# Performance work log

Hardware: AMD Instinct MI355X
Metric: run time of the kernel (lower is better)

The kernel has to match this reference:

```python
import jax, jax.numpy as jnp
import numpy as np

H = W = 512
P = H * W          # total superpixel member pixels
N_SP = 1024        # number of superpixels


def _conv(x, w, b):
    # x: [N,C,H,W], w: [O,I,3,3] -> [N,O,H,W], SAME padding
    y = jax.lax.conv_general_dilated(
        x, w, window_strides=(1, 1), padding='SAME',
        dimension_numbers=('NCHW', 'OIHW', 'NCHW'))
    return y + b[None, :, None, None]


def _embed(raw, w1, b1, w2, b2, w3, b3):
    h = jax.nn.relu(_conv(raw, w1, b1))
    h = jax.nn.relu(_conv(h, w2, b2))
    return _conv(h, w3, b3)  # [1, 10, H, W]


def setup_inputs() -> dict:
    key = jax.random.key(0)
    ks = jax.random.split(key, 6)
    raw = jax.random.normal(ks[0], (1, 1, H, W), dtype=jnp.float32)
    w1 = jax.random.normal(ks[1], (64, 1, 3, 3), dtype=jnp.float32) * 0.3
    b1 = jnp.zeros((64,), jnp.float32)
    w2 = jax.random.normal(ks[2], (64, 64, 3, 3), dtype=jnp.float32) * 0.05
    b2 = jnp.zeros((64,), jnp.float32)
    w3 = jax.random.normal(ks[3], (10, 64, 3, 3), dtype=jnp.float32) * 0.05
    b3 = jnp.zeros((10,), jnp.float32)
    pix_rc = jax.random.randint(ks[4], (P, 2), 0, H, dtype=jnp.int32)
    seg_ids = jax.random.randint(ks[5], (P,), 0, N_SP, dtype=jnp.int32)
    return {"raw": raw, "w1": w1, "b1": b1, "w2": w2, "b2": b2,
            "w3": w3, "b3": b3, "pix_rc": pix_rc, "seg_ids": seg_ids,
            "n_sp": N_SP}


def reference(raw, w1, b1, w2, b2, w3, b3, pix_rc, seg_ids, n_sp):
    feats = _embed(raw, w1, b1, w2, b2, w3, b3)  # [1, C, H, W]
    f = feats[0]                                  # [C, H, W]
    # gather per-pixel feature vectors: [P, C]
    vals = f[:, pix_rc[:, 0], pix_rc[:, 1]].T
    # scatter-mean over superpixels (= per-sp sum / mass)
    sums = jax.ops.segment_sum(vals, seg_ids, num_segments=n_sp)      # [n_sp, C]
    cnts = jax.ops.segment_sum(jnp.ones((vals.shape[0],), vals.dtype),
                               seg_ids, num_segments=n_sp)            # [n_sp]
    return sums / jnp.maximum(cnts, 1.0)[:, None]
```

## Files before the change

### kernel.cpp

```cpp
#include <hip/hip_runtime.h>

typedef __attribute__((ext_vector_type(8))) short short8;
typedef __attribute__((ext_vector_type(4))) float f32x4;

constexpr int H = 512, W = 512;
constexpr int P = H * W;
constexpr int NSP = 1024;
constexpr int SBLK = 512;
constexpr int FGRP = 16;

__device__ inline unsigned short f2bf(float f) {
  unsigned u = __builtin_bit_cast(unsigned, f);
  unsigned r = (u + 0x7fffu + ((u >> 16) & 1u)) >> 16;
  return (unsigned short)r;
}
__device__ inline float bflo(unsigned u) { return __builtin_bit_cast(float, u << 16); }
__device__ inline float bfhi(unsigned u) { return __builtin_bit_cast(float, u & 0xffff0000u); }

__device__ inline int xcd_swz(int b, int cpx) { return (b & 7) * cpx + (b >> 3); }

__global__ __launch_bounds__(256) void prep_k(const float* __restrict__ w2,
                                              const float* __restrict__ w3,
                                              unsigned short* __restrict__ wt2s,
                                              unsigned short* __restrict__ wt3s,
                                              unsigned short* __restrict__ zeros) {
  if (blockIdx.x == 0 && threadIdx.x < 128) zeros[threadIdx.x] = 0;
  int i = blockIdx.x * 256 + threadIdx.x;
  if (i < 36864) {
    int k = i >> 11;
    int t = (i >> 3) & 255;
    int e = i & 7;
    int r = t >> 2, sp = t & 3, s = sp ^ ((r >> 2) & 3);
    int tap = k >> 1, ic = (k & 1) * 32 + s * 8 + e;
    wt2s[i] = f2bf(w2[r * 576 + ic * 9 + tap]);
  } else if (i < 46080) {
    int j = i - 36864;
    int k = j >> 9;
    int t = (j >> 3) & 63;
    int e = j & 7;
    int r = t >> 2, sp = t & 3, s = sp ^ ((r >> 2) & 3);
    int tap = k >> 1, ic = (k & 1) * 32 + s * 8 + e;
    wt3s[j] = (r < 10) ? f2bf(w3[r * 576 + ic * 9 + tap]) : (unsigned short)0;
  }
}

__global__ __launch_bounds__(512) void conv2_k(const float* __restrict__ raw,
                                               const float* __restrict__ w1,
                                               const float* __restrict__ b1,
                                               const unsigned short* __restrict__ wts,
                                               const float* __restrict__ bias,
                                               unsigned short* __restrict__ ynhwc) {
  constexpr int DCS = 4096;
  __shared__ __align__(16) unsigned short acts[352 * 64];
  __shared__ __align__(16) unsigned short wbuf[3 * DCS];
  __shared__ unsigned short rawtb[12 * 36 + 4];
  int tid = threadIdx.x;
  int lane = tid & 63, wave = tid >> 6;
  int logical = xcd_swz(blockIdx.x, 128);
  int tilex = logical & 15, tiley = logical >> 4;
  int c0 = tilex * 32, r0 = tiley * 8;

#pragma unroll
  for (int k0 = 0; k0 < 2; ++k0) {
    const unsigned short* src = wts + (size_t)k0 * DCS + tid * 8;
    unsigned short* dstb = wbuf + k0 * DCS + wave * 512;
    __builtin_amdgcn_global_load_lds((const __attribute__((address_space(1))) void*)src,
                                     (__attribute__((address_space(3))) void*)dstb, 16, 0, 0);
  }
  if (tid < 432) {
    int rr = tid / 36, cc = tid - rr * 36;
    int gr = r0 + rr - 2, gc = c0 + cc - 2;
    bool ok = ((unsigned)gr < 512u) && ((unsigned)gc < 512u);
    rawtb[tid] = ok ? f2bf(raw[gr * 512 + gc]) : (unsigned short)0;
  }

  int q = lane >> 4, n = lane & 15;
  int og1 = wave & 3;
  short8 a1f;
  {
    short av[8];
#pragma unroll
    for (int e = 0; e < 8; ++e) av[e] = 0;
    int oc = og1 * 16 + n;
    if (q == 0) {
#pragma unroll
      for (int e = 0; e < 8; ++e) av[e] = (short)f2bf(w1[oc * 9 + e]);
    } else if (q == 1) {
      av[0] = (short)f2bf(w1[oc * 9 + 8]);
    }
    a1f = (short8){av[0], av[1], av[2], av[3], av[4], av[5], av[6], av[7]};
  }
  float bb1[4];
#pragma unroll
  for (int r2 = 0; r2 < 4; ++r2) bb1[r2] = b1[og1 * 16 + q * 4 + r2];
  __syncthreads();

  char* actw = (char*)acts;
  int tbase = (wave < 4) ? 0 : 11;
  for (int ti = 0; ti < 11; ++ti) {
    int t = tbase + ti;
    int px = t * 16 + n;
    bool okp = px < 340;
    int prow = px / 34, pcol = px - prow * 34;
    int prc = okp ? prow : 9;
    short bv[8];
#pragma unroll
    for (int e = 0; e < 8; ++e) bv[e] = 0;
    if (q == 0) {
#pragma unroll
      for (int e = 0; e < 8; ++e) {
        int dy = e / 3, dx = e - dy * 3;
        bv[e] = (short)rawtb[(prc + dy) * 36 + pcol + dx];
      }
    } else if (q == 1) {
      bv[0] = (short)rawtb[(prc + 2) * 36 + pcol + 2];
    }
    short8 b1f = (short8){bv[0], bv[1], bv[2], bv[3], bv[4], bv[5], bv[6], bv[7]};
    f32x4 d = __builtin_amdgcn_mfma_f32_16x16x32_bf16(a1f, b1f,
                                                       (f32x4){0.f, 0.f, 0.f, 0.f}, 0, 0, 0);
    int gr1 = r0 + prow - 1, gc1 = c0 + pcol - 1;
    bool ok1 = okp && ((unsigned)gr1 < 512u) && ((unsigned)gc1 < 512u);
    float o0 = ok1 ? fmaxf(d.x + bb1[0], 0.f) : 0.f;
    float o1 = ok1 ? fmaxf(d.y + bb1[1], 0.f) : 0.f;
    float o2 = ok1 ? fmaxf(d.z + bb1[2], 0.f) : 0.f;
    float o3 = ok1 ? fmaxf(d.w + bb1[3], 0.f) : 0.f;
    unsigned lo = (unsigned)f2bf(o0) | ((unsigned)f2bf(o1) << 16);
    unsigned hi = (unsigned)f2bf(o2) | ((unsigned)f2bf(o3) << 16);
    int wa = px * 128 + ((((og1 * 2 + (q >> 1)) ^ (px & 7)) << 4)) + ((q & 1) << 3);
    *reinterpret_cast<uint2*>(actw + wa) = make_uint2(lo, hi);
  }
  __syncthreads();

  f32x4 acc[4][2];
#pragma unroll
  for (int og = 0; og < 4; ++og)
#pragma unroll
    for (int g = 0; g < 2; ++g) acc[og][g] = (f32x4){0.f, 0.f, 0.f, 0.f};

  int plbase[2];
#pragma unroll
  for (int g = 0; g < 2; ++g) plbase[g] = wave * 34 + 16 * g + n;
  const char* actb = (const char*)acts;

#pragma unroll
  for (int j = 0; j < 9; ++j) {
    if (j == 8) {
      asm volatile("s_waitcnt vmcnt(0)" ::: "memory");
    } else {
      asm volatile("s_waitcnt vmcnt(1)" ::: "memory");
    }
    __builtin_amdgcn_sched_barrier(0);
    __builtin_amdgcn_s_barrier();
    __builtin_amdgcn_sched_barrier(0);
    if (j + 2 < 9) {
      const unsigned short* src = wts + (size_t)(j + 2) * DCS + tid * 8;
      unsigned short* dstb = wbuf + ((j + 2) % 3) * DCS + wave * 512;
      __builtin_amdgcn_global_load_lds((const __attribute__((address_space(1))) void*)src,
                                       (__attribute__((address_space(3))) void*)dstb, 16, 0, 0);
    }
    const int kyy = j / 3, kxx = j - kyy * 3;
    const char* sb = (const char*)(wbuf + (j % 3) * DCS);
#pragma unroll
    for (int kc = 0; kc < 2; ++kc) {
      const char* wb = sb + kc * 4096;
      short8 af[4];
#pragma unroll
      for (int og = 0; og < 4; ++og) {
        int r = og * 16 + n;
        af[og] = *reinterpret_cast<const short8*>(wb + r * 64 + ((q ^ ((r >> 2) & 3)) * 16));
      }
#pragma unroll
      for (int g = 0; g < 2; ++g) {
        int pl = plbase[g] + kyy * 34 + kxx;
        int addr = pl * 128 + (((kc * 4 + q) ^ (pl & 7)) * 16);
        short8 bf = *reinterpret_cast<const short8*>(actb + addr);
#pragma unroll
        for (int og = 0; og < 4; ++og)
          acc[og][g] = __builtin_amdgcn_mfma_f32_16x16x32_bf16(af[og], bf, acc[og][g], 0, 0, 0);
      }
    }
  }

  __syncthreads();
  char* ob = (char*)acts;
#pragma unroll
  for (int og = 0; og < 4; ++og) {
    float b0 = bias[og * 16 + q * 4 + 0], b1v = bias[og * 16 + q * 4 + 1];
    float b2 = bias[og * 16 + q * 4 + 2], b3 = bias[og * 16 + q * 4 + 3];
#pragma unroll
    for (int g = 0; g < 2; ++g) {
      int pl = wave * 32 + g * 16 + n;
      f32x4 v = acc[og][g];
      float o0 = fmaxf(v.x + b0, 0.f), o1 = fmaxf(v.y + b1v, 0.f);
      float o2 = fmaxf(v.z + b2, 0.f), o3 = fmaxf(v.w + b3, 0.f);
      unsigned lo = (unsigned)f2bf(o0) | ((unsigned)f2bf(o1) << 16);
      unsigned hi = (unsigned)f2bf(o2) | ((unsigned)f2bf(o3) << 16);
      int lslot = og * 2 + (q >> 1);
      int wa = pl * 128 + (((lslot ^ (pl & 7)) << 4)) + ((q & 1) << 3);
      *reinterpret_cast<uint2*>(ob + wa) = make_uint2(lo, hi);
    }
  }
  __syncthreads();
  char* yb = (char*)ynhwc;
#pragma unroll
  for (int it = 0; it < 4; ++it) {
    int c = it * 512 + tid;
    int pl = c >> 3, slot = c & 7;
    uint4 v = *reinterpret_cast<const uint4*>(ob + pl * 128 + ((slot ^ (pl & 7)) << 4));
    size_t gb = (((size_t)(r0 + (pl >> 5)) * 512) + c0 + (pl & 31)) * 128 + slot * 16;
    *reinterpret_cast<uint4*>(yb + gb) = v;
  }
}

__global__ __launch_bounds__(512) void conv3_k(const unsigned short* __restrict__ xin,
                                               const unsigned short* __restrict__ wts,
                                               const float* __restrict__ bias,
                                               unsigned short* __restrict__ feats,
                                               const unsigned short* __restrict__ zeros) {
  __shared__ __align__(16) unsigned short acts[352 * 64];
  __shared__ __align__(16) unsigned short wl[9216];
  int tid = threadIdx.x;
  int lane = tid & 63, wave = tid >> 6;
  int logical = xcd_swz(blockIdx.x, 128);
  int tilex = logical & 15, tiley = logical >> 4;
  int c0 = tilex * 32, r0 = tiley * 8;

  for (int wi = wave; wi < 18; wi += 8) {
    const unsigned short* src = wts + (size_t)wi * 512 + lane * 8;
    unsigned short* dstb = &wl[wi * 512];
    __builtin_amdgcn_global_load_lds((const __attribute__((address_space(1))) void*)src,
                                     (__attribute__((address_space(3))) void*)dstb, 16, 0, 0);
  }
  for (int wi = wave; wi < 44; wi += 8) {
    int cidx = wi * 64 + lane;
    int pix = cidx >> 3, slotp = cidx & 7;
    int prow = pix / 34, pcol = pix - prow * 34;
    int gr = r0 + prow - 1, gc = c0 + pcol - 1;
    int slot = slotp ^ (pix & 7);
    bool ok = (pix < 340) & ((unsigned)gr < 512u) & ((unsigned)gc < 512u);
    const unsigned short* src = ok ? (xin + (((size_t)(gr * 512 + gc)) << 6) + slot * 8) : zeros;
    unsigned short* dstb = &acts[wi * 512];
    __builtin_amdgcn_global_load_lds((const __attribute__((address_space(1))) void*)src,
                                     (__attribute__((address_space(3))) void*)dstb, 16, 0, 0);
  }
  __syncthreads();

  int q = lane >> 4, n = lane & 15;
  f32x4 acc[2];
#pragma unroll
  for (int g = 0; g < 2; ++g) acc[g] = (f32x4){0.f, 0.f, 0.f, 0.f};
  int plbase[2];
#pragma unroll
  for (int g = 0; g < 2; ++g) plbase[g] = wave * 34 + 16 * g + n;
  const char* actb = (const char*)acts;
  const char* wb0 = (const char*)wl;

#pragma unroll
  for (int k = 0; k < 18; ++k) {
    const int tap = k >> 1, kc = k & 1;
    const int kyy = tap / 3, kxx = tap - kyy * 3;
    short8 af = *reinterpret_cast<const short8*>(wb0 + k * 1024 + n * 64 +
                                                 ((q ^ ((n >> 2) & 3)) * 16));
#pragma unroll
    for (int g = 0; g < 2; ++g) {
      int pl = plbase[g] + kyy * 34 + kxx;
      int addr = pl * 128 + (((kc * 4 + q) ^ (pl & 7)) * 16);
      short8 bf = *reinterpret_cast<const short8*>(actb + addr);
      acc[g] = __builtin_amdgcn_mfma_f32_16x16x32_bf16(af, bf, acc[g], 0, 0, 0);
    }
  }

  __syncthreads();
  char* ob = (char*)acts;
  float bb[4];
#pragma unroll
  for (int r2 = 0; r2 < 4; ++r2) {
    int oc = q * 4 + r2;
    bb[r2] = (oc < 10) ? bias[oc] : 0.f;
  }
#pragma unroll
  for (int g = 0; g < 2; ++g) {
    int pl = wave * 32 + g * 16 + n;
    f32x4 v = acc[g];
    float o0 = v.x + bb[0], o1 = v.y + bb[1], o2 = v.z + bb[2], o3 = v.w + bb[3];
    if (q < 2) {
      unsigned u0 = (unsigned)f2bf(o0) | ((unsigned)f2bf(o1) << 16);
      unsigned u1 = (unsigned)f2bf(o2) | ((unsigned)f2bf(o3) << 16);
      *reinterpret_cast<uint2*>(ob + pl * 24 + q * 8) = make_uint2(u0, u1);
    } else if (q == 2) {
      *reinterpret_cast<unsigned*>(ob + pl * 24 + 16) =
          (unsigned)f2bf(o0) | ((unsigned)f2bf(o1) << 16);
    }
  }
  __syncthreads();
  char* fb = (char*)feats;
#pragma unroll
  for (int it = 0; it < 3; ++it) {
    int c = it * 512 + tid;
    if (c < 1280) {
      int row = c / 160, wb = c - row * 160;
      int byte = wb * 4;
      int px = byte / 20, off = byte - px * 20;
      unsigned v = *reinterpret_cast<const unsigned*>(ob + (row * 32 + px) * 24 + off);
      size_t gbyte = (((size_t)(r0 + row) * 512) + c0) * 20 + (size_t)byte;
      *reinterpret_cast<unsigned*>(fb + gbyte) = v;
    }
  }
}

__global__ __launch_bounds__(512) void scatter_k(const unsigned short* __restrict__ feats,
                                                 const int* __restrict__ pix_rc,
                                                 const int* __restrict__ seg,
                                                 float* __restrict__ partials) {
  __shared__ float ls[NSP * 10];
  __shared__ float lc[NSP];
  int tid = threadIdx.x;
  for (int i = tid; i < NSP * 10; i += 512) ls[i] = 0.f;
  for (int i = tid; i < NSP; i += 512) lc[i] = 0.f;
  __syncthreads();

  constexpr int PER = P / SBLK;
  int p0 = blockIdx.x * PER;
  for (int p = p0 + tid; p < p0 + PER; p += 512) {
    int2 rc = *reinterpret_cast<const int2*>(pix_rc + 2 * p);
    int s = seg[p];
    size_t gpix = (size_t)rc.x * 512 + rc.y;
    const char* fp = (const char*)feats + gpix * 20;
    uint4 a = *reinterpret_cast<const uint4*>(fp);
    unsigned e = *reinterpret_cast<const unsigned*>(fp + 16);
    float v[10];
    v[0] = bflo(a.x); v[1] = bfhi(a.x);
    v[2] = bflo(a.y); v[3] = bfhi(a.y);
    v[4] = bflo(a.z); v[5] = bfhi(a.z);
    v[6] = bflo(a.w); v[7] = bfhi(a.w);
    v[8] = bflo(e);   v[9] = bfhi(e);
#pragma unroll
    for (int ch = 0; ch < 10; ++ch) atomicAdd(&ls[s * 10 + ch], v[ch]);
    atomicAdd(&lc[s], 1.f);
  }
  __syncthreads();

  float* outp = partials + (size_t)blockIdx.x * (NSP * 11);
  for (int i = tid; i < NSP * 10; i += 512) outp[i] = ls[i];
  for (int i = tid; i < NSP; i += 512) outp[NSP * 10 + i] = lc[i];
}

__global__ __launch_bounds__(256) void finA_k(const float* __restrict__ partials,
                                              float* __restrict__ partials2) {
  int g = blockIdx.x / 44;
  int e = (blockIdx.x - g * 44) * 256 + threadIdx.x;
  const float* base = partials + (size_t)(g * 32) * (NSP * 11) + e;
  float s = 0.f;
#pragma unroll 8
  for (int k = 0; k < 32; ++k) s += base[(size_t)k * (NSP * 11)];
  partials2[(size_t)g * (NSP * 11) + e] = s;
}

__global__ __launch_bounds__(256) void finB_k(const float* __restrict__ partials2,
                                              float* __restrict__ out) {
  int i = blockIdx.x * 256 + threadIdx.x;
  if (i >= NSP * 10) return;
  int sp = i / 10;
  float s = 0.f, cnt = 0.f;
#pragma unroll
  for (int g = 0; g < FGRP; ++g) {
    const float* pp = partials2 + (size_t)g * (NSP * 11);
    s += pp[i];
    cnt += pp[NSP * 10 + sp];
  }
  out[i] = s / fmaxf(cnt, 1.f);
}

extern "C" void kernel_launch(void* const* d_in, const int* in_sizes, int n_in,
                              void* d_out, int out_size, void* d_ws, size_t ws_size,
                              hipStream_t stream) {
  const float* raw = (const float*)d_in[0];
  const float* w1  = (const float*)d_in[1];
  const float* b1  = (const float*)d_in[2];
  const float* w2  = (const float*)d_in[3];
  const float* b2  = (const float*)d_in[4];
  const float* w3  = (const float*)d_in[5];
  const float* b3  = (const float*)d_in[6];
  const int* pix_rc = (const int*)d_in[7];
  const int* seg    = (const int*)d_in[8];
  float* out = (float*)d_out;

  char* ws = (char*)d_ws;
  float* partials  = (float*)(ws + 0);
  float* partials2 = (float*)(ws + 23068672);
  unsigned short* h2    = (unsigned short*)(ws + 25165824);
  unsigned short* feats = (unsigned short*)(ws + 58720256);
  unsigned short* wt2s  = (unsigned short*)(ws + 63963136);
  unsigned short* wt3s  = (unsigned short*)(ws + 64036864);
  unsigned short* zeros = (unsigned short*)(ws + 64055296);

  prep_k<<<180, 256, 0, stream>>>(w2, w3, wt2s, wt3s, zeros);
  conv2_k<<<1024, 512, 0, stream>>>(raw, w1, b1, wt2s, b2, h2);
  conv3_k<<<1024, 512, 0, stream>>>(h2, wt3s, b3, feats, zeros);
  scatter_k<<<SBLK, 512, 0, stream>>>(feats, pix_rc, seg, partials);
  finA_k<<<FGRP * 44, 256, 0, stream>>>(partials, partials2);
  finB_k<<<40, 256, 0, stream>>>(partials2, out);
}
```

Before: 80.25 us.

## Read conv weights directly from global memory instead of staging in LDS

Removes the LDS weight buffers and the triple-buffered async weight pipeline, including its per-tap barriers, in both conv kernels. Each wave now loads its MFMA A-fragments straight from global memory, and the prep kernel drops the XOR swizzle since no LDS bank layout is needed. It also raises launch bounds to a minimum of 6 blocks per CU, using the freed LDS to fit more resident blocks. The cost is redundant global/L2 weight reads by every wave, with latency exposed in the MFMA loop, and possible register pressure from the occupancy hint.

```diff
diff --git a/kernel.cpp b/kernel.cpp
--- a/kernel.cpp
+++ b/kernel.cpp
@@ -30,7 +30,7 @@
     int k = i >> 11;
     int t = (i >> 3) & 255;
     int e = i & 7;
-    int r = t >> 2, sp = t & 3, s = sp ^ ((r >> 2) & 3);
+    int r = t >> 2, s = t & 3;
     int tap = k >> 1, ic = (k & 1) * 32 + s * 8 + e;
     wt2s[i] = f2bf(w2[r * 576 + ic * 9 + tap]);
   } else if (i < 46080) {
@@ -38,21 +38,19 @@
     int k = j >> 9;
     int t = (j >> 3) & 63;
     int e = j & 7;
-    int r = t >> 2, sp = t & 3, s = sp ^ ((r >> 2) & 3);
+    int r = t >> 2, s = t & 3;
     int tap = k >> 1, ic = (k & 1) * 32 + s * 8 + e;
     wt3s[j] = (r < 10) ? f2bf(w3[r * 576 + ic * 9 + tap]) : (unsigned short)0;
   }
 }
 
-__global__ __launch_bounds__(512) void conv2_k(const float* __restrict__ raw,
-                                               const float* __restrict__ w1,
-                                               const float* __restrict__ b1,
-                                               const unsigned short* __restrict__ wts,
-                                               const float* __restrict__ bias,
-                                               unsigned short* __restrict__ ynhwc) {
-  constexpr int DCS = 4096;
+__global__ __launch_bounds__(512, 6) void conv2_k(const float* __restrict__ raw,
+                                                  const float* __restrict__ w1,
+                                                  const float* __restrict__ b1,
+                                                  const unsigned short* __restrict__ wts,
+                                                  const float* __restrict__ bias,
+                                                  unsigned short* __restrict__ ynhwc) {
   __shared__ __align__(16) unsigned short acts[352 * 64];
-  __shared__ __align__(16) unsigned short wbuf[3 * DCS];
   __shared__ unsigned short rawtb[12 * 36 + 4];
   int tid = threadIdx.x;
   int lane = tid & 63, wave = tid >> 6;
@@ -60,13 +58,6 @@
   int tilex = logical & 15, tiley = logical >> 4;
   int c0 = tilex * 32, r0 = tiley * 8;
 
-#pragma unroll
-  for (int k0 = 0; k0 < 2; ++k0) {
-    const unsigned short* src = wts + (size_t)k0 * DCS + tid * 8;
-    unsigned short* dstb = wbuf + k0 * DCS + wave * 512;
-    __builtin_amdgcn_global_load_lds((const __attribute__((address_space(1))) void*)src,
-                                     (__attribute__((address_space(3))) void*)dstb, 16, 0, 0);
-  }
   if (tid < 432) {
     int rr = tid / 36, cc = tid - rr * 36;
     int gr = r0 + rr - 2, gc = c0 + cc - 2;
@@ -144,30 +135,15 @@
 
 #pragma unroll
   for (int j = 0; j < 9; ++j) {
-    if (j == 8) {
-      asm volatile("s_waitcnt vmcnt(0)" ::: "memory");
-    } else {
-      asm volatile("s_waitcnt vmcnt(1)" ::: "memory");
-    }
-    __builtin_amdgcn_sched_barrier(0);
-    __builtin_amdgcn_s_barrier();
-    __builtin_amdgcn_sched_barrier(0);
-    if (j + 2 < 9) {
-      const unsigned short* src = wts + (size_t)(j + 2) * DCS + tid * 8;
-      unsigned short* dstb = wbuf + ((j + 2) % 3) * DCS + wave * 512;
-      __builtin_amdgcn_global_load_lds((const __attribute__((address_space(1))) void*)src,
-                                       (__attribute__((address_space(3))) void*)dstb, 16, 0, 0);
-    }
     const int kyy = j / 3, kxx = j - kyy * 3;
-    const char* sb = (const char*)(wbuf + (j % 3) * DCS);
 #pragma unroll
     for (int kc = 0; kc < 2; ++kc) {
-      const char* wb = sb + kc * 4096;
+      const int k = j * 2 + kc;
       short8 af[4];
 #pragma unroll
       for (int og = 0; og < 4; ++og) {
-        int r = og * 16 + n;
-        af[og] = *reinterpret_cast<const short8*>(wb + r * 64 + ((q ^ ((r >> 2) & 3)) * 16));
+        const unsigned short* ap = wts + (size_t)k * 2048 + (og * 16 + n) * 32 + q * 8;
+        af[og] = *reinterpret_cast<const short8*>(ap);
       }
 #pragma unroll
       for (int g = 0; g < 2; ++g) {
@@ -212,25 +188,18 @@
   }
 }
 
-__global__ __launch_bounds__(512) void conv3_k(const unsigned short* __restrict__ xin,
-                                               const unsigned short* __restrict__ wts,
-                                               const float* __restrict__ bias,
-                                               unsigned short* __restrict__ feats,
-                                               const unsigned short* __restrict__ zeros) {
+__global__ __launch_bounds__(512, 6) void conv3_k(const unsigned short* __restrict__ xin,
+                                                  const unsigned short* __restrict__ wts,
+                                                  const float* __restrict__ bias,
+                                                  unsigned short* __restrict__ feats,
+                                                  const unsigned short* __restrict__ zeros) {
   __shared__ __align__(16) unsigned short acts[352 * 64];
-  __shared__ __align__(16) unsigned short wl[9216];
   int tid = threadIdx.x;
   int lane = tid & 63, wave = tid >> 6;
   int logical = xcd_swz(blockIdx.x, 128);
   int tilex = logical & 15, tiley = logical >> 4;
   int c0 = tilex * 32, r0 = tiley * 8;
 
-  for (int wi = wave; wi < 18; wi += 8) {
-    const unsigned short* src = wts + (size_t)wi * 512 + lane * 8;
-    unsigned short* dstb = &wl[wi * 512];
-    __builtin_amdgcn_global_load_lds((const __attribute__((address_space(1))) void*)src,
-                                     (__attribute__((address_space(3))) void*)dstb, 16, 0, 0);
-  }
   for (int wi = wave; wi < 44; wi += 8) {
     int cidx = wi * 64 + lane;
     int pix = cidx >> 3, slotp = cidx & 7;
@@ -253,14 +222,12 @@
 #pragma unroll
   for (int g = 0; g < 2; ++g) plbase[g] = wave * 34 + 16 * g + n;
   const char* actb = (const char*)acts;
-  const char* wb0 = (const char*)wl;
 
 #pragma unroll
   for (int k = 0; k < 18; ++k) {
     const int tap = k >> 1, kc = k & 1;
     const int kyy = tap / 3, kxx = tap - kyy * 3;
-    short8 af = *reinterpret_cast<const short8*>(wb0 + k * 1024 + n * 64 +
-                                                 ((q ^ ((n >> 2) & 3)) * 16));
+    short8 af = *reinterpret_cast<const short8*>(wts + (size_t)k * 512 + n * 32 + q * 8);
 #pragma unroll
     for (int g = 0; g < 2; ++g) {
       int pl = plbase[g] + kyy * 34 + kxx;
```

After: 101.2 us. +26.1%, slower.

## Replace per-block LDS histograms with global atomics into 16 replicated copies

Applied to the files above, without the earlier changes.

The scatter kernel no longer builds a full 1024x11 LDS histogram per block and writes 512 partial copies. Each thread instead atomically adds its pixel's features directly into one of 16 global copies, chosen by block index, which prep_k now zeroes. This removes the LDS init and flush, the large partials buffer, and the finA reduction kernel. In exchange it relies on global float atomics, with contention spread across 16 copies, and the order of float summation changes.

```diff
diff --git a/kernel.cpp b/kernel.cpp
--- a/kernel.cpp
+++ b/kernel.cpp
@@ -6,8 +6,8 @@
 constexpr int H = 512, W = 512;
 constexpr int P = H * W;
 constexpr int NSP = 1024;
-constexpr int SBLK = 512;
-constexpr int FGRP = 16;
+constexpr int NCOPY = 16;
+constexpr int PROW = NSP * 11;
 
 __device__ inline unsigned short f2bf(float f) {
   unsigned u = __builtin_bit_cast(unsigned, f);
@@ -23,9 +23,11 @@
                                               const float* __restrict__ w3,
                                               unsigned short* __restrict__ wt2s,
                                               unsigned short* __restrict__ wt3s,
-                                              unsigned short* __restrict__ zeros) {
+                                              unsigned short* __restrict__ zeros,
+                                              float* __restrict__ p2) {
   if (blockIdx.x == 0 && threadIdx.x < 128) zeros[threadIdx.x] = 0;
   int i = blockIdx.x * 256 + threadIdx.x;
+  for (int z = i; z < NCOPY * PROW; z += 180 * 256) p2[z] = 0.f;
   if (i < 36864) {
     int k = i >> 11;
     int t = (i >> 3) & 255;
@@ -308,63 +310,38 @@
   }
 }
 
-__global__ __launch_bounds__(512) void scatter_k(const unsigned short* __restrict__ feats,
+__global__ __launch_bounds__(256) void scatter_k(const unsigned short* __restrict__ feats,
                                                  const int* __restrict__ pix_rc,
                                                  const int* __restrict__ seg,
-                                                 float* __restrict__ partials) {
-  __shared__ float ls[NSP * 10];
-  __shared__ float lc[NSP];
-  int tid = threadIdx.x;
-  for (int i = tid; i < NSP * 10; i += 512) ls[i] = 0.f;
-  for (int i = tid; i < NSP; i += 512) lc[i] = 0.f;
-  __syncthreads();
-
-  constexpr int PER = P / SBLK;
-  int p0 = blockIdx.x * PER;
-  for (int p = p0 + tid; p < p0 + PER; p += 512) {
-    int2 rc = *reinterpret_cast<const int2*>(pix_rc + 2 * p);
-    int s = seg[p];
-    size_t gpix = (size_t)rc.x * 512 + rc.y;
-    const char* fp = (const char*)feats + gpix * 20;
-    uint4 a = *reinterpret_cast<const uint4*>(fp);
-    unsigned e = *reinterpret_cast<const unsigned*>(fp + 16);
-    float v[10];
-    v[0] = bflo(a.x); v[1] = bfhi(a.x);
-    v[2] = bflo(a.y); v[3] = bfhi(a.y);
-    v[4] = bflo(a.z); v[5] = bfhi(a.z);
-    v[6] = bflo(a.w); v[7] = bfhi(a.w);
-    v[8] = bflo(e);   v[9] = bfhi(e);
-#pragma unroll
-    for (int ch = 0; ch < 10; ++ch) atomicAdd(&ls[s * 10 + ch], v[ch]);
-    atomicAdd(&lc[s], 1.f);
-  }
-  __syncthreads();
-
-  float* outp = partials + (size_t)blockIdx.x * (NSP * 11);
-  for (int i = tid; i < NSP * 10; i += 512) outp[i] = ls[i];
-  for (int i = tid; i < NSP; i += 512) outp[NSP * 10 + i] = lc[i];
-}
-
-__global__ __launch_bounds__(256) void finA_k(const float* __restrict__ partials,
-                                              float* __restrict__ partials2) {
-  int g = blockIdx.x / 44;
-  int e = (blockIdx.x - g * 44) * 256 + threadIdx.x;
-  const float* base = partials + (size_t)(g * 32) * (NSP * 11) + e;
-  float s = 0.f;
-#pragma unroll 8
-  for (int k = 0; k < 32; ++k) s += base[(size_t)k * (NSP * 11)];
-  partials2[(size_t)g * (NSP * 11) + e] = s;
-}
-
-__global__ __launch_bounds__(256) void finB_k(const float* __restrict__ partials2,
+                                                 float* __restrict__ p2) {
+  int p = blockIdx.x * 256 + threadIdx.x;
+  float* dst = p2 + (size_t)(blockIdx.x & (NCOPY - 1)) * PROW;
+  int2 rc = *reinterpret_cast<const int2*>(pix_rc + 2 * p);
+  int s = seg[p];
+  size_t gpix = (size_t)rc.x * 512 + rc.y;
+  const char* fp = (const char*)feats + gpix * 20;
+  uint4 a = *reinterpret_cast<const uint4*>(fp);
+  unsigned e = *reinterpret_cast<const unsigned*>(fp + 16);
+  float v[10];
+  v[0] = bflo(a.x); v[1] = bfhi(a.x);
+  v[2] = bflo(a.y); v[3] = bfhi(a.y);
+  v[4] = bflo(a.z); v[5] = bfhi(a.z);
+  v[6] = bflo(a.w); v[7] = bfhi(a.w);
+  v[8] = bflo(e);   v[9] = bfhi(e);
+#pragma unroll
+  for (int ch = 0; ch < 10; ++ch) atomicAdd(&dst[s * 10 + ch], v[ch]);
+  atomicAdd(&dst[NSP * 10 + s], 1.f);
+}
+
+__global__ __launch_bounds__(256) void finB_k(const float* __restrict__ p2,
                                               float* __restrict__ out) {
   int i = blockIdx.x * 256 + threadIdx.x;
   if (i >= NSP * 10) return;
   int sp = i / 10;
   float s = 0.f, cnt = 0.f;
 #pragma unroll
-  for (int g = 0; g < FGRP; ++g) {
-    const float* pp = partials2 + (size_t)g * (NSP * 11);
+  for (int g = 0; g < NCOPY; ++g) {
+    const float* pp = p2 + (size_t)g * PROW;
     s += pp[i];
     cnt += pp[NSP * 10 + sp];
   }
@@ -386,18 +363,16 @@
   float* out = (float*)d_out;
 
   char* ws = (char*)d_ws;
-  float* partials  = (float*)(ws + 0);
-  float* partials2 = (float*)(ws + 23068672);
+  float* p2 = (float*)(ws + 0);
   unsigned short* h2    = (unsigned short*)(ws + 25165824);
   unsigned short* feats = (unsigned short*)(ws + 58720256);
   unsigned short* wt2s  = (unsigned short*)(ws + 63963136);
   unsigned short* wt3s  = (unsigned short*)(ws + 64036864);
   unsigned short* zeros = (unsigned short*)(ws + 64055296);
 
-  prep_k<<<180, 256, 0, stream>>>(w2, w3, wt2s, wt3s, zeros);
+  prep_k<<<180, 256, 0, stream>>>(w2, w3, wt2s, wt3s, zeros, p2);
   conv2_k<<<1024, 512, 0, stream>>>(raw, w1, b1, wt2s, b2, h2);
   conv3_k<<<1024, 512, 0, stream>>>(h2, wt3s, b3, feats, zeros);
-  scatter_k<<<SBLK, 512, 0, stream>>>(feats, pix_rc, seg, partials);
-  finA_k<<<FGRP * 44, 256, 0, stream>>>(partials, partials2);
-  finB_k<<<40, 256, 0, stream>>>(partials2, out);
-}
+  scatter_k<<<1024, 256, 0, stream>>>(feats, pix_rc, seg, p2);
+  finB_k<<<40, 256, 0, stream>>>(p2, out);
+}
```

After: 202.6 us. +152.5%, slower.
